# Kernel optimization log

Hardware: AMD Instinct MI355X
Metric: run time of the kernel (lower is better)

## Reference

```python
import jax, jax.numpy as jnp
from jax import lax
import numpy as np

T, B, D, H = 512, 256, 128, 256
SHIFT = 0.0


def setup_inputs() -> dict:
    key = jax.random.key(0)
    ks = jax.random.split(key, 11)
    s_in = 1.0 / np.sqrt(D + H)
    s_cl = 1.0 / np.sqrt(H)
    return {
        "inputs": jax.random.normal(ks[0], (T, B, D), dtype=jnp.float32),
        "Wf": jax.random.normal(ks[1], (H, D + H), dtype=jnp.float32) * s_in,
        "bf": jax.random.normal(ks[2], (H,), dtype=jnp.float32) * s_in,
        "Wi": jax.random.normal(ks[3], (H, D + H), dtype=jnp.float32) * s_in,
        "bi": jax.random.normal(ks[4], (H,), dtype=jnp.float32) * s_in,
        "Wg": jax.random.normal(ks[5], (H, D + H), dtype=jnp.float32) * s_in,
        "bg": jax.random.normal(ks[6], (H,), dtype=jnp.float32) * s_in,
        "Wo": jax.random.normal(ks[7], (H, D + H), dtype=jnp.float32) * s_in,
        "bo": jax.random.normal(ks[8], (H,), dtype=jnp.float32) * s_in,
        "Wc": jax.random.normal(ks[9], (1, H), dtype=jnp.float32) * s_cl,
        "bc": jax.random.normal(ks[10], (1,), dtype=jnp.float32) * s_cl,
    }


def reference(inputs, Wf, bf, Wi, bi, Wg, bg, Wo, bo, Wc, bc):
    # Fuse the four gate linears into one GEMM per step: [4H, D+H]
    W = jnp.concatenate([Wf, Wi, Wg, Wo], axis=0)
    b = jnp.concatenate([bf, bi, bg, bo], axis=0)
    h = W.shape[0] // 4
    batch = inputs.shape[1]

    def step(carry, x):
        hx, cx = carry
        combined = jnp.concatenate([x, hx], axis=1)      # [B, D+H]
        z = combined @ W.T + b                            # [B, 4H]
        f = jax.nn.sigmoid(z[:, 0 * h:1 * h])
        i = jax.nn.sigmoid(z[:, 1 * h:2 * h])
        g = jnp.tanh(z[:, 2 * h:3 * h])
        o = jax.nn.sigmoid(z[:, 3 * h:4 * h])
        cx = f * cx + i * g
        hx = o * jnp.tanh(cx)
        return (hx, cx), hx

    h0 = jnp.zeros((batch, h), dtype=inputs.dtype)
    c0 = jnp.zeros((batch, h), dtype=inputs.dtype)
    (hx, cx), hs = lax.scan(step, (h0, c0), inputs)       # hs: [T, B, H]

    logits = hs @ Wc.T + bc                               # [T, B, 1]
    probs = jax.nn.sigmoid(logits + SHIFT)
    return (jnp.concatenate([probs, 1.0 - probs], axis=-1), hx, cx)
```

## Files before the change

kernel.cpp:

```cpp
#include <hip/hip_runtime.h>
#include <hip/hip_bf16.h>


#define T_STEPS 512
#define BATCH   256
#define DIN     128
#define HID     256
#define KDIM    384
#define LDK     392
#define GRIDN   256

typedef __attribute__((ext_vector_type(8))) short short8;
typedef __attribute__((ext_vector_type(4))) short short4v;
typedef __attribute__((ext_vector_type(4))) float f32x4;

__device__ __forceinline__ unsigned short f2bf(float f) {
    unsigned u = __float_as_uint(f);
    unsigned r = (u + 0x7FFFu + ((u >> 16) & 1u)) >> 16;
    return (unsigned short)r;
}
__device__ __forceinline__ float bf2f(unsigned short s) {
    return __uint_as_float(((unsigned)s) << 16);
}
__device__ __forceinline__ float sigmoid_f(float x) {
    return 1.f / (1.f + __expf(-x));
}
__device__ __forceinline__ float tanh_f(float x) {
    float e = __expf(2.f * x);
    return 1.f - 2.f / (e + 1.f);
}
__device__ __forceinline__ void poll_load64(const unsigned int* p, uint4& a,
                                            uint4& b, uint4& c, uint4& d) {
    asm volatile(
        "global_load_dwordx4 %0, %4, off sc1\n\t"
        "global_load_dwordx4 %1, %4, off offset:16 sc1\n\t"
        "global_load_dwordx4 %2, %4, off offset:32 sc1\n\t"
        "global_load_dwordx4 %3, %4, off offset:48 sc1\n\t"
        "s_waitcnt vmcnt(0)"
        : "=&v"(a), "=&v"(b), "=&v"(c), "=&v"(d)
        : "v"(p)
        : "memory");
}
__device__ __forceinline__ void store_sc1_u32(unsigned int* p, unsigned int v) {
    asm volatile("global_store_dword %0, %1, off sc1" :: "v"(p), "v"(v) : "memory");
}
__device__ __forceinline__ unsigned pack2bf(unsigned lo, unsigned hi) {
    return (hi & 0xFFFF0000u) | (lo >> 16);
}

__global__ __launch_bounds__(256) void pack_w(
    const float* __restrict__ Wf, const float* __restrict__ Wi,
    const float* __restrict__ Wg, const float* __restrict__ Wo,
    unsigned short* __restrict__ Wp) {
    int idx = blockIdx.x * 256 + threadIdx.x;
    int n = idx / KDIM;
    int k = idx - n * KDIM;
    int g = n >> 8, j = n & 255;
    const float* s = (g == 0) ? Wf : (g == 1) ? Wi : (g == 2) ? Wg : Wo;
    Wp[idx] = f2bf(s[j * KDIM + k]);
}

__global__ __launch_bounds__(256) void pack_b(
    const float* __restrict__ bf, const float* __restrict__ bi,
    const float* __restrict__ bg, const float* __restrict__ bo,
    float* __restrict__ bp) {
    int n = blockIdx.x * 256 + threadIdx.x;
    int g = n >> 8, j = n & 255;
    const float* s = (g == 0) ? bf : (g == 1) ? bi : (g == 2) ? bg : bo;
    bp[n] = s[j];
}

__global__ __launch_bounds__(256) void init_k(unsigned int* __restrict__ hxp) {
    int tid = blockIdx.x * 256 + threadIdx.x;
    hxp[tid] = 0u;
    hxp[65536 + tid] = 0u;
}

__global__ __launch_bounds__(256, 1) void lstm_persist(
    const float* __restrict__ X,
    const unsigned short* __restrict__ W,
    const float* __restrict__ bias,
    unsigned int* __restrict__ hxp,
    unsigned short* __restrict__ hist,
    float* __restrict__ out) {
    __shared__ __align__(16) unsigned short W_s[64 * LDK];
    __shared__ __align__(16) unsigned short comb_s[16 * LDK];
    __shared__ __align__(16) float z_s[4 * 272];

    const int tid = threadIdx.x;
    const int bg = blockIdx.x >> 4, jg = blockIdx.x & 15;
    const int b0 = bg * 16, j0 = jg * 16;
    const int wave = tid >> 6, lane = tid & 63;
    const int l16 = lane & 15, quad = lane >> 4;
    const int bi = tid >> 4, jj = tid & 15;
    const int b = b0 + bi, j = j0 + jj;

#pragma unroll
    for (int c = 0; c < 12; ++c) {
        int q = c * 256 + tid;
        int row = q / 48, c8 = q - row * 48;
        int g = row >> 4, jr = row & 15;
        short8 v = *(const short8*)(W + ((g * 256 + j0 + jr) * KDIM + c8 * 8));
        *(short8*)(&W_s[row * LDK + c8 * 8]) = v;
    }
    const float bs0 = bias[0 * HID + j];
    const float bs1 = bias[1 * HID + j];
    const float bs2 = bias[2 * HID + j];
    const float bs3 = bias[3 * HID + j];

    float c_reg = 0.f;
    float h_final = 0.f;

    const unsigned short* arow = &comb_s[l16 * LDK + quad * 8];
    const unsigned short* brow = &W_s[(wave * 16 + l16) * LDK + quad * 8];
    const int hrow = tid >> 4, hc = tid & 15;
    const int xr0 = tid >> 5, xc4 = tid & 31, xr1 = (tid + 256) >> 5;

    const float* xb = X + b0 * DIN;
    float4 xv0 = *(const float4*)(xb + xr0 * DIN + xc4 * 4);
    float4 xv1 = *(const float4*)(xb + xr1 * DIN + xc4 * 4);

    __syncthreads();

    for (int k = 0; k < T_STEPS; ++k) {
        {
            short4v r;
            r.x = (short)f2bf(xv0.x); r.y = (short)f2bf(xv0.y);
            r.z = (short)f2bf(xv0.z); r.w = (short)f2bf(xv0.w);
            *(short4v*)(&comb_s[xr0 * LDK + xc4 * 4]) = r;
            r.x = (short)f2bf(xv1.x); r.y = (short)f2bf(xv1.y);
            r.z = (short)f2bf(xv1.z); r.w = (short)f2bf(xv1.w);
            *(short4v*)(&comb_s[xr1 * LDK + xc4 * 4]) = r;
        }

        const unsigned int* hbase =
            hxp + (k & 1) * 65536 + (b0 + hrow) * HID + hc * 16;
        uint4 a, bq, cq, d;
        const unsigned tag = (unsigned)k;
        for (;;) {
            poll_load64(hbase, a, bq, cq, d);
            bool fresh =
                ((a.x  ^ tag) & 0xFFFFu) == 0 && ((a.y  ^ tag) & 0xFFFFu) == 0 &&
                ((a.z  ^ tag) & 0xFFFFu) == 0 && ((a.w  ^ tag) & 0xFFFFu) == 0 &&
                ((bq.x ^ tag) & 0xFFFFu) == 0 && ((bq.y ^ tag) & 0xFFFFu) == 0 &&
                ((bq.z ^ tag) & 0xFFFFu) == 0 && ((bq.w ^ tag) & 0xFFFFu) == 0 &&
                ((cq.x ^ tag) & 0xFFFFu) == 0 && ((cq.y ^ tag) & 0xFFFFu) == 0 &&
                ((cq.z ^ tag) & 0xFFFFu) == 0 && ((cq.w ^ tag) & 0xFFFFu) == 0 &&
                ((d.x  ^ tag) & 0xFFFFu) == 0 && ((d.y  ^ tag) & 0xFFFFu) == 0 &&
                ((d.z  ^ tag) & 0xFFFFu) == 0 && ((d.w  ^ tag) & 0xFFFFu) == 0;
            if (__all(fresh)) break;
            __builtin_amdgcn_s_sleep(2);
        }
        {
            uint4 p0, p1;
            p0.x = pack2bf(a.x, a.y);  p0.y = pack2bf(a.z, a.w);
            p0.z = pack2bf(bq.x, bq.y); p0.w = pack2bf(bq.z, bq.w);
            p1.x = pack2bf(cq.x, cq.y); p1.y = pack2bf(cq.z, cq.w);
            p1.z = pack2bf(d.x, d.y);  p1.w = pack2bf(d.z, d.w);
            *(uint4*)(&comb_s[hrow * LDK + DIN + hc * 16]) = p0;
            *(uint4*)(&comb_s[hrow * LDK + DIN + hc * 16 + 8]) = p1;
        }
        __syncthreads();

        f32x4 acc0 = {0.f, 0.f, 0.f, 0.f}, acc1 = {0.f, 0.f, 0.f, 0.f};
#pragma unroll
        for (int kt = 0; kt < 6; ++kt) {
            short8 a0 = *(const short8*)(arow + (2 * kt) * 32);
            short8 b0v = *(const short8*)(brow + (2 * kt) * 32);
            short8 a1 = *(const short8*)(arow + (2 * kt + 1) * 32);
            short8 b1v = *(const short8*)(brow + (2 * kt + 1) * 32);
            acc0 = __builtin_amdgcn_mfma_f32_16x16x32_bf16(a0, b0v, acc0, 0, 0, 0);
            acc1 = __builtin_amdgcn_mfma_f32_16x16x32_bf16(a1, b1v, acc1, 0, 0, 0);
        }
#pragma unroll
        for (int r = 0; r < 4; ++r)
            z_s[wave * 272 + (quad * 4 + r) * 17 + l16] = acc0[r] + acc1[r];
        __syncthreads();

        if (k + 1 < T_STEPS) {
            const float* xn = X + (size_t)(k + 1) * BATCH * DIN + b0 * DIN;
            xv0 = *(const float4*)(xn + xr0 * DIN + xc4 * 4);
            xv1 = *(const float4*)(xn + xr1 * DIN + xc4 * 4);
        }

        float zf = z_s[0 * 272 + bi * 17 + jj] + bs0;
        float zi = z_s[1 * 272 + bi * 17 + jj] + bs1;
        float zg = z_s[2 * 272 + bi * 17 + jj] + bs2;
        float zo = z_s[3 * 272 + bi * 17 + jj] + bs3;
        float fg = sigmoid_f(zf);
        float ig = sigmoid_f(zi);
        float gg = tanh_f(zg);
        float og = sigmoid_f(zo);
        c_reg = fg * c_reg + ig * gg;
        float hval = og * tanh_f(c_reg);
        unsigned short hb = f2bf(hval);
        hist[(size_t)k * BATCH * HID + b * HID + j] = hb;
        store_sc1_u32(hxp + ((k + 1) & 1) * 65536 + b * HID + j,
                      ((unsigned)hb << 16) | (unsigned)(k + 1));
        if (k == T_STEPS - 1) h_final = hval;
    }

    out[T_STEPS * BATCH * 2 + b * HID + j] = h_final;
    out[T_STEPS * BATCH * 2 + BATCH * HID + b * HID + j] = c_reg;
}

__global__ __launch_bounds__(256) void probs_k(
    const unsigned short* __restrict__ hist, const float* __restrict__ Wc,
    const float* __restrict__ bc, float* __restrict__ out) {
    const int wave = threadIdx.x >> 6, lane = threadIdx.x & 63;
    const size_t row = (size_t)blockIdx.x * 4 + wave;
    const unsigned short* h = hist + row * HID;
    short4v hv = *(const short4v*)(h + lane * 4);
    const float4 wv = *(const float4*)(Wc + lane * 4);
    float p = bf2f((unsigned short)hv.x) * wv.x + bf2f((unsigned short)hv.y) * wv.y +
              bf2f((unsigned short)hv.z) * wv.z + bf2f((unsigned short)hv.w) * wv.w;
#pragma unroll
    for (int off = 32; off >= 1; off >>= 1) p += __shfl_down(p, off);
    if (lane == 0) {
        float prob = 1.f / (1.f + __expf(-(p + bc[0])));
        out[row * 2]     = prob;
        out[row * 2 + 1] = 1.f - prob;
    }
}

extern "C" void kernel_launch(void* const* d_in, const int* in_sizes, int n_in,
                              void* d_out, int out_size, void* d_ws, size_t ws_size,
                              hipStream_t stream) {
    const float* X  = (const float*)d_in[0];
    const float* Wf = (const float*)d_in[1];
    const float* bfp= (const float*)d_in[2];
    const float* Wi = (const float*)d_in[3];
    const float* bip= (const float*)d_in[4];
    const float* Wg = (const float*)d_in[5];
    const float* bgp= (const float*)d_in[6];
    const float* Wo = (const float*)d_in[7];
    const float* bop= (const float*)d_in[8];
    const float* Wc = (const float*)d_in[9];
    const float* bc = (const float*)d_in[10];
    float* out = (float*)d_out;

    char* ws = (char*)d_ws;
    unsigned short* Wpack = (unsigned short*)(ws);
    float* bias = (float*)(ws + 786432);
    unsigned int* hxp = (unsigned int*)(ws + 790528);
    unsigned short* hist = (unsigned short*)(ws + 1314816);

    pack_w<<<1536, 256, 0, stream>>>(Wf, Wi, Wg, Wo, Wpack);
    pack_b<<<4, 256, 0, stream>>>(bfp, bip, bgp, bop, bias);
    init_k<<<256, 256, 0, stream>>>(hxp);

    void* kargs[6] = {(void*)&X, (void*)&Wpack, (void*)&bias,
                      (void*)&hxp, (void*)&hist, (void*)&out};
    hipLaunchCooperativeKernel((const void*)lstm_persist, dim3(GRIDN), dim3(256),
                               kargs, 0, stream);

    probs_k<<<32768, 256, 0, stream>>>(hist, Wc, bc, out);
}
```

Measured before the change: 1.304 ms.

## Add fast sc0 polling path with sc1 fallback buffer for hidden-state exchange

Hidden-state words are now written twice: a plain store into a fast buffer and an sc1 store into a second buffer. Consumers first poll the fast buffer with sc0 loads for a bounded number of tries, and permanently fall back to sleeping sc1 polling of the second buffer if a timeout occurs. Block-to-tile mapping is swapped so batch groups vary fastest, which may place producers and consumers within the same XCD or L2. The next-step X prefetch is moved after the stores. This aims to cut cross-CU synchronization latency per step, at the cost of double stores and a reliance on cache-visibility behavior.

```diff
diff --git a/kernel.cpp b/kernel.cpp
--- a/kernel.cpp
+++ b/kernel.cpp
@@ -9,6 +9,7 @@
 #define KDIM    384
 #define LDK     392
 #define GRIDN   256
+#define NPOLL   96
 
 typedef __attribute__((ext_vector_type(8))) short short8;
 typedef __attribute__((ext_vector_type(4))) short short4v;
@@ -29,23 +30,46 @@
     float e = __expf(2.f * x);
     return 1.f - 2.f / (e + 1.f);
 }
-__device__ __forceinline__ void poll_load64(const unsigned int* p, uint4& a,
-                                            uint4& b, uint4& c, uint4& d) {
+__device__ __forceinline__ void poll_load_sc0(const unsigned int* p, uint4& a,
+                                              uint4& b, uint4& c, uint4& d) {
+    asm volatile(
+        "global_load_dwordx4 %0, %4, off sc0\n\t"
+        "global_load_dwordx4 %1, %4, off offset:16 sc0\n\t"
+        "global_load_dwordx4 %2, %4, off offset:32 sc0\n\t"
+        "global_load_dwordx4 %3, %4, off offset:48 sc0\n\t"
+        "s_waitcnt vmcnt(0)"
+        : "=&v"(a), "=&v"(b), "=&v"(c), "=&v"(d) : "v"(p) : "memory");
+}
+__device__ __forceinline__ void poll_load_sc1(const unsigned int* p, uint4& a,
+                                              uint4& b, uint4& c, uint4& d) {
     asm volatile(
         "global_load_dwordx4 %0, %4, off sc1\n\t"
         "global_load_dwordx4 %1, %4, off offset:16 sc1\n\t"
         "global_load_dwordx4 %2, %4, off offset:32 sc1\n\t"
         "global_load_dwordx4 %3, %4, off offset:48 sc1\n\t"
         "s_waitcnt vmcnt(0)"
-        : "=&v"(a), "=&v"(b), "=&v"(c), "=&v"(d)
-        : "v"(p)
-        : "memory");
+        : "=&v"(a), "=&v"(b), "=&v"(c), "=&v"(d) : "v"(p) : "memory");
+}
+__device__ __forceinline__ void store_plain_u32(unsigned int* p, unsigned int v) {
+    asm volatile("global_store_dword %0, %1, off" :: "v"(p), "v"(v) : "memory");
 }
 __device__ __forceinline__ void store_sc1_u32(unsigned int* p, unsigned int v) {
     asm volatile("global_store_dword %0, %1, off sc1" :: "v"(p), "v"(v) : "memory");
 }
 __device__ __forceinline__ unsigned pack2bf(unsigned lo, unsigned hi) {
     return (hi & 0xFFFF0000u) | (lo >> 16);
+}
+__device__ __forceinline__ bool tags_ok(const uint4& a, const uint4& b,
+                                        const uint4& c, const uint4& d,
+                                        unsigned tag) {
+    return ((a.x ^ tag) & 0xFFFFu) == 0 && ((a.y ^ tag) & 0xFFFFu) == 0 &&
+           ((a.z ^ tag) & 0xFFFFu) == 0 && ((a.w ^ tag) & 0xFFFFu) == 0 &&
+           ((b.x ^ tag) & 0xFFFFu) == 0 && ((b.y ^ tag) & 0xFFFFu) == 0 &&
+           ((b.z ^ tag) & 0xFFFFu) == 0 && ((b.w ^ tag) & 0xFFFFu) == 0 &&
+           ((c.x ^ tag) & 0xFFFFu) == 0 && ((c.y ^ tag) & 0xFFFFu) == 0 &&
+           ((c.z ^ tag) & 0xFFFFu) == 0 && ((c.w ^ tag) & 0xFFFFu) == 0 &&
+           ((d.x ^ tag) & 0xFFFFu) == 0 && ((d.y ^ tag) & 0xFFFFu) == 0 &&
+           ((d.z ^ tag) & 0xFFFFu) == 0 && ((d.w ^ tag) & 0xFFFFu) == 0;
 }
 
 __global__ __launch_bounds__(256) void pack_w(
@@ -74,6 +98,8 @@
     int tid = blockIdx.x * 256 + threadIdx.x;
     hxp[tid] = 0u;
     hxp[65536 + tid] = 0u;
+    hxp[131072 + tid] = 0u;
+    hxp[196608 + tid] = 0u;
 }
 
 __global__ __launch_bounds__(256, 1) void lstm_persist(
@@ -86,9 +112,10 @@
     __shared__ __align__(16) unsigned short W_s[64 * LDK];
     __shared__ __align__(16) unsigned short comb_s[16 * LDK];
     __shared__ __align__(16) float z_s[4 * 272];
+    __shared__ int fastok_s;
 
     const int tid = threadIdx.x;
-    const int bg = blockIdx.x >> 4, jg = blockIdx.x & 15;
+    const int bg = blockIdx.x & 15, jg = blockIdx.x >> 4;
     const int b0 = bg * 16, j0 = jg * 16;
     const int wave = tid >> 6, lane = tid & 63;
     const int l16 = lane & 15, quad = lane >> 4;
@@ -107,6 +134,7 @@
     const float bs1 = bias[1 * HID + j];
     const float bs2 = bias[2 * HID + j];
     const float bs3 = bias[3 * HID + j];
+    if (tid == 0) fastok_s = 1;
 
     float c_reg = 0.f;
     float h_final = 0.f;
@@ -123,6 +151,13 @@
     __syncthreads();
 
     for (int k = 0; k < T_STEPS; ++k) {
+        const unsigned tag = (unsigned)k;
+        const unsigned int* fb =
+            hxp + (k & 1) * 65536 + (b0 + hrow) * HID + hc * 16;
+        const unsigned int* sb = fb + 131072;
+        uint4 a, bq, cq, d;
+        const int usefast = fastok_s;
+
         {
             short4v r;
             r.x = (short)f2bf(xv0.x); r.y = (short)f2bf(xv0.y);
@@ -133,30 +168,36 @@
             *(short4v*)(&comb_s[xr1 * LDK + xc4 * 4]) = r;
         }
 
-        const unsigned int* hbase =
-            hxp + (k & 1) * 65536 + (b0 + hrow) * HID + hc * 16;
-        uint4 a, bq, cq, d;
-        const unsigned tag = (unsigned)k;
-        for (;;) {
-            poll_load64(hbase, a, bq, cq, d);
-            bool fresh =
-                ((a.x  ^ tag) & 0xFFFFu) == 0 && ((a.y  ^ tag) & 0xFFFFu) == 0 &&
-                ((a.z  ^ tag) & 0xFFFFu) == 0 && ((a.w  ^ tag) & 0xFFFFu) == 0 &&
-                ((bq.x ^ tag) & 0xFFFFu) == 0 && ((bq.y ^ tag) & 0xFFFFu) == 0 &&
-                ((bq.z ^ tag) & 0xFFFFu) == 0 && ((bq.w ^ tag) & 0xFFFFu) == 0 &&
-                ((cq.x ^ tag) & 0xFFFFu) == 0 && ((cq.y ^ tag) & 0xFFFFu) == 0 &&
-                ((cq.z ^ tag) & 0xFFFFu) == 0 && ((cq.w ^ tag) & 0xFFFFu) == 0 &&
-                ((d.x  ^ tag) & 0xFFFFu) == 0 && ((d.y  ^ tag) & 0xFFFFu) == 0 &&
-                ((d.z  ^ tag) & 0xFFFFu) == 0 && ((d.w  ^ tag) & 0xFFFFu) == 0;
-            if (__all(fresh)) break;
-            __builtin_amdgcn_s_sleep(2);
-        }
+        if (usefast) {
+            int tries = NPOLL;
+            bool ok = false;
+            for (;;) {
+                poll_load_sc0(fb, a, bq, cq, d);
+                if (tags_ok(a, bq, cq, d, tag)) { ok = true; break; }
+                if (--tries == 0) break;
+            }
+            if (!ok) {
+                fastok_s = 0;
+                for (;;) {
+                    poll_load_sc1(sb, a, bq, cq, d);
+                    if (tags_ok(a, bq, cq, d, tag)) break;
+                    __builtin_amdgcn_s_sleep(1);
+                }
+            }
+        } else {
+            for (;;) {
+                poll_load_sc1(sb, a, bq, cq, d);
+                if (tags_ok(a, bq, cq, d, tag)) break;
+                __builtin_amdgcn_s_sleep(1);
+            }
+        }
+
         {
             uint4 p0, p1;
-            p0.x = pack2bf(a.x, a.y);  p0.y = pack2bf(a.z, a.w);
+            p0.x = pack2bf(a.x, a.y);   p0.y = pack2bf(a.z, a.w);
             p0.z = pack2bf(bq.x, bq.y); p0.w = pack2bf(bq.z, bq.w);
             p1.x = pack2bf(cq.x, cq.y); p1.y = pack2bf(cq.z, cq.w);
-            p1.z = pack2bf(d.x, d.y);  p1.w = pack2bf(d.z, d.w);
+            p1.z = pack2bf(d.x, d.y);   p1.w = pack2bf(d.z, d.w);
             *(uint4*)(&comb_s[hrow * LDK + DIN + hc * 16]) = p0;
             *(uint4*)(&comb_s[hrow * LDK + DIN + hc * 16 + 8]) = p1;
         }
@@ -176,12 +217,6 @@
         for (int r = 0; r < 4; ++r)
             z_s[wave * 272 + (quad * 4 + r) * 17 + l16] = acc0[r] + acc1[r];
         __syncthreads();
-
-        if (k + 1 < T_STEPS) {
-            const float* xn = X + (size_t)(k + 1) * BATCH * DIN + b0 * DIN;
-            xv0 = *(const float4*)(xn + xr0 * DIN + xc4 * 4);
-            xv1 = *(const float4*)(xn + xr1 * DIN + xc4 * 4);
-        }
 
         float zf = z_s[0 * 272 + bi * 17 + jj] + bs0;
         float zi = z_s[1 * 272 + bi * 17 + jj] + bs1;
@@ -194,10 +229,18 @@
         c_reg = fg * c_reg + ig * gg;
         float hval = og * tanh_f(c_reg);
         unsigned short hb = f2bf(hval);
+        unsigned int hword = ((unsigned)hb << 16) | (unsigned)(k + 1);
+        unsigned int* fdst = hxp + ((k + 1) & 1) * 65536 + b * HID + j;
+        store_plain_u32(fdst, hword);
+        store_sc1_u32(fdst + 131072, hword);
         hist[(size_t)k * BATCH * HID + b * HID + j] = hb;
-        store_sc1_u32(hxp + ((k + 1) & 1) * 65536 + b * HID + j,
-                      ((unsigned)hb << 16) | (unsigned)(k + 1));
-        if (k == T_STEPS - 1) h_final = hval;
+        if (k + 1 < T_STEPS) {
+            const float* xn = X + (size_t)(k + 1) * BATCH * DIN + b0 * DIN;
+            xv0 = *(const float4*)(xn + xr0 * DIN + xc4 * 4);
+            xv1 = *(const float4*)(xn + xr1 * DIN + xc4 * 4);
+        } else {
+            h_final = hval;
+        }
     }
 
     out[T_STEPS * BATCH * 2 + b * HID + j] = h_final;
@@ -243,7 +286,7 @@
     unsigned short* Wpack = (unsigned short*)(ws);
     float* bias = (float*)(ws + 786432);
     unsigned int* hxp = (unsigned int*)(ws + 790528);
-    unsigned short* hist = (unsigned short*)(ws + 1314816);
+    unsigned short* hist = (unsigned short*)(ws + 1839104);
 
     pack_w<<<1536, 256, 0, stream>>>(Wf, Wi, Wg, Wo, Wpack);
     pack_b<<<4, 256, 0, stream>>>(bfp, bip, bgp, bop, bias);
@@ -251,8 +294,8 @@
 
     void* kargs[6] = {(void*)&X, (void*)&Wpack, (void*)&bias,
                       (void*)&hxp, (void*)&hist, (void*)&out};
-    hipLaunchCooperativeKernel((const void*)lstm_persist, dim3(GRIDN), dim3(256),
-                               kargs, 0, stream);
+    (void)hipLaunchCooperativeKernel((const void*)lstm_persist, dim3(GRIDN),
+                                     dim3(256), kargs, 0, stream);
 
     probs_k<<<32768, 256, 0, stream>>>(hist, Wc, bc, out);
 }
```

New measurement: 1.183 ms. -9.3%, faster.
